# Kernel tuning notes

Hardware: AMD Instinct MI355X
Metric: run time of the kernel (lower is better)

The kernel has to match this reference:

```python
import jax, jax.numpy as jnp
import numpy as np

N = 1048576   # total nodes
B = 32768     # number of graphs
F = 128       # input_dim
STEPS = 6


def setup_inputs() -> dict:
    key = jax.random.key(0)
    k0, k1, k2, k3, k4 = jax.random.split(key, 5)
    s = 1.0 / np.sqrt(F)  # torch LSTM init scale
    x = jax.random.normal(k0, (N, F), dtype=jnp.float32)
    # equal-sized, sorted graph assignment so every graph is non-empty
    batch = (jnp.arange(N, dtype=jnp.int64) * B) // N
    W_ih = jax.random.uniform(k1, (4 * F, 2 * F), jnp.float32, -s, s)
    W_hh = jax.random.uniform(k2, (4 * F, F), jnp.float32, -s, s)
    b_ih = jax.random.uniform(k3, (4 * F,), jnp.float32, -s, s)
    b_hh = jax.random.uniform(k4, (4 * F,), jnp.float32, -s, s)
    return {"x": x, "batch": batch, "W_ih": W_ih, "W_hh": W_hh,
            "b_ih": b_ih, "b_hh": b_hh}


def _lstm_cell(x_in, h, c, W_ih, W_hh, b_ih, b_hh):
    # torch gate order: i, f, g, o
    gates = x_in @ W_ih.T + h @ W_hh.T + b_ih + b_hh  # [B, 4F]
    i, f, g, o = jnp.split(gates, 4, axis=-1)
    c_new = jax.nn.sigmoid(f) * c + jax.nn.sigmoid(i) * jnp.tanh(g)
    h_new = jax.nn.sigmoid(o) * jnp.tanh(c_new)
    return h_new, c_new


def reference(x, batch, W_ih, W_hh, b_ih, b_hh):
    # Vectorized set2set: each graph's batch-1 LSTM is independent, so we run
    # all B graphs' LSTMs as one batched cell, and do the softmax-attention
    # readout with segment ops over the ragged node sets.
    h = jnp.zeros((B, F), x.dtype)
    c = jnp.zeros((B, F), x.dtype)
    q_star = jnp.zeros((B, 2 * F), x.dtype)
    batch = batch.astype(jnp.int32)
    for _ in range(STEPS):
        q, c = _lstm_cell(q_star, h, c, W_ih, W_hh, b_ih, b_hh)  # [B, F]
        h = q
        e = jnp.sum(x * q[batch], axis=-1)  # [N] attention logits
        # per-graph stable softmax
        emax = jax.ops.segment_max(e, batch, num_segments=B)
        ee = jnp.exp(e - emax[batch])
        denom = jax.ops.segment_sum(ee, batch, num_segments=B)
        a = ee / denom[batch]  # [N]
        r = jax.ops.segment_sum(a[:, None] * x, batch, num_segments=B)  # [B, F]
        q_star = jnp.concatenate([q, r], axis=-1)  # [B, 2F]
    return q_star
```

## Files before the change

kernel.cpp:

```cpp
#include <hip/hip_runtime.h>
#include <hip/hip_bf16.h>
#include <hip/hip_fp16.h>
#include <cstdint>


#define NSTEPS   6
#define NSEG     32768
#define NCHUNK   32768
#define MAXC     8
#define XSH      136
#define MTHREADS 1024
#define MGRID    256
#define ESHIFT   20.0f

typedef _Float16 half2_t __attribute__((ext_vector_type(2)));

__device__ __forceinline__ float sigmoidf_(float v) {
    return 1.0f / (1.0f + __expf(-v));
}

__device__ __forceinline__ float fdot2_(unsigned int w, unsigned int q, float acc) {
    return __builtin_amdgcn_fdot2(__builtin_bit_cast(half2_t, w),
                                  __builtin_bit_cast(half2_t, q), acc, false);
}

__device__ __forceinline__ void lgkm_barrier() {
    asm volatile("s_waitcnt lgkmcnt(0)" ::: "memory");
    __builtin_amdgcn_s_barrier();
    asm volatile("" ::: "memory");
}

__global__ void pack_weights_kernel(const float* __restrict__ Wih,
                                    const float* __restrict__ Whh,
                                    const float* __restrict__ bih,
                                    const float* __restrict__ bhh,
                                    float* __restrict__ wtp,
                                    float* __restrict__ b4) {
    const int k = blockIdx.x;
    const int f = threadIdx.x;
    float w[4];
    #pragma unroll
    for (int j = 0; j < 4; ++j) {
        const int row = j * 128 + f;
        float v = Wih[row * 256 + k];
        if (k < 128) v += Whh[row * 128 + k];
        w[j] = v;
    }
    float4 wv; wv.x = w[0]; wv.y = w[1]; wv.z = w[2]; wv.w = w[3];
    reinterpret_cast<float4*>(wtp)[k * 128 + f] = wv;
    if (k == 0) {
        float4 bv;
        bv.x = bih[0 * 128 + f] + bhh[0 * 128 + f];
        bv.y = bih[1 * 128 + f] + bhh[1 * 128 + f];
        bv.z = bih[2 * 128 + f] + bhh[2 * 128 + f];
        bv.w = bih[3 * 128 + f] + bhh[3 * 128 + f];
        reinterpret_cast<float4*>(b4)[f] = bv;
    }
}

__global__ void pack_f16_kernel(const float* __restrict__ wtp,
                                uint4* __restrict__ wph) {
    const int p = blockIdx.x;
    const int f = threadIdx.x;
    const float4 w0 = reinterpret_cast<const float4*>(wtp)[(2 * p) * 128 + f];
    const float4 w1 = reinterpret_cast<const float4*>(wtp)[(2 * p + 1) * 128 + f];
    __half2 h[4];
    h[0] = __floats2half2_rn(w0.x, w1.x);
    h[1] = __floats2half2_rn(w0.y, w1.y);
    h[2] = __floats2half2_rn(w0.z, w1.z);
    h[3] = __floats2half2_rn(w0.w, w1.w);
    wph[p * 128 + f] = *reinterpret_cast<uint4*>(h);
}

__global__ void zero_kernel(int* __restrict__ p, int n) {
    for (int i = blockIdx.x * blockDim.x + threadIdx.x; i < n;
         i += gridDim.x * blockDim.x) p[i] = 0;
}

__global__ void seg_count_kernel(const int* __restrict__ batch,
                                 int* __restrict__ counts) {
    const int c = blockIdx.x * blockDim.x + threadIdx.x;
    if (c < NCHUNK) {
        const int v = batch[c * 32];
        if (v >= 0 && v < NSEG)
            atomicAdd(&counts[v], 1);
    }
}

__global__ __launch_bounds__(1024)
void scan_kernel(const int* __restrict__ counts,
                 int* __restrict__ offs, int* __restrict__ cursor,
                 int* __restrict__ activeList, int* __restrict__ nActive) {
    __shared__ int sc[1024];
    const int t = threadIdx.x;
    const int base = t * 32;
    int local[32];
    int sum = 0;
    #pragma unroll
    for (int j = 0; j < 32; ++j) { local[j] = counts[base + j]; sum += local[j]; }
    sc[t] = sum;
    __syncthreads();
    for (int d = 1; d < 1024; d <<= 1) {
        const int v = (t >= d) ? sc[t - d] : 0;
        __syncthreads();
        sc[t] += v;
        __syncthreads();
    }
    int run = sc[t] - sum;
    for (int j = 0; j < 32; ++j) {
        const int s = base + j;
        offs[s] = run;
        cursor[s] = run;
        if (local[j] > 0) {
            const int idx = atomicAdd(nActive, 1);
            activeList[idx] = s;
        }
        run += local[j];
    }
}

__global__ void fill_kernel(const int* __restrict__ batch,
                            int* __restrict__ cursor,
                            int* __restrict__ chunk_list) {
    const int c = blockIdx.x * blockDim.x + threadIdx.x;
    if (c < NCHUNK) {
        const int v = batch[c * 32];
        if (v >= 0 && v < NSEG) {
            const int pos = atomicAdd(&cursor[v], 1);
            chunk_list[pos] = c;
        }
    }
}

__global__ __launch_bounds__(128)
void empty_traj_kernel(const float* __restrict__ wtp,
                       const float* __restrict__ b4,
                       float* __restrict__ qe,
                       float* __restrict__ qe01) {
    __shared__ float q_s[128];
    const int f = threadIdx.x;
    const float4 bb = reinterpret_cast<const float4*>(b4)[f];
    q_s[f] = 0.0f;
    float c = 0.0f;
    __syncthreads();
    for (int step = 0; step < NSTEPS; ++step) {
        float a0 = 0.f, a1 = 0.f, a2 = 0.f, a3 = 0.f;
        for (int k = 0; k < 128; ++k) {
            const float4 w = reinterpret_cast<const float4*>(wtp)[k * 128 + f];
            const float qv = q_s[k];
            a0 = fmaf(w.x, qv, a0); a1 = fmaf(w.y, qv, a1);
            a2 = fmaf(w.z, qv, a2); a3 = fmaf(w.w, qv, a3);
        }
        __syncthreads();
        c = sigmoidf_(a1 + bb.y) * c + sigmoidf_(a0 + bb.x) * tanhf(a2 + bb.z);
        const float qv = sigmoidf_(a3 + bb.w) * tanhf(c);
        q_s[f] = qv;
        if (step == 0) { qe01[f] = qv; qe01[128 + f] = c; }
        __syncthreads();
    }
    qe[f] = q_s[f];
}

__global__ void bcast_empty_kernel(const int* __restrict__ counts,
                                   const float* __restrict__ qe,
                                   float* __restrict__ out) {
    const int lane = threadIdx.x & 63;
    const int wave0 = (blockIdx.x * blockDim.x + threadIdx.x) >> 6;
    const int nwave = (gridDim.x * blockDim.x) >> 6;
    float4 v = make_float4(0.f, 0.f, 0.f, 0.f);
    if (lane < 32) v = reinterpret_cast<const float4*>(qe)[lane];
    for (int s = wave0; s < NSEG; s += nwave) {
        if (counts[s] != 0) continue;
        reinterpret_cast<float4*>(out)[(size_t)s * 64 + lane] = v;
    }
}

__global__ __launch_bounds__(MTHREADS)
void main_seg_kernel(const float* __restrict__ x,
                     const uint4* __restrict__ wph,
                     const float* __restrict__ b4,
                     const float* __restrict__ qe01,
                     const int* __restrict__ counts,
                     const int* __restrict__ offs,
                     const int* __restrict__ chunk_list,
                     const int* __restrict__ activeList,
                     const int* __restrict__ nActive,
                     float* __restrict__ out) {
    __shared__ __align__(16) __half x_h[2][256][XSH];
    __shared__ __align__(16) __half q_h[2][2][256];
    __shared__ __align__(16) float  e_s[2][256];
    __shared__ __align__(16) float  rpart_s[2][8][128];
    __shared__ float dsum_s[16];
    __shared__ int   clist_s[2][MAXC];
    __shared__ int   cnt_s[2];

    const int t  = threadIdx.x;
    const int ko = t & 7;
    const int f  = t >> 3;
    const float4 bb = reinterpret_cast<const float4*>(b4)[f];
    const float c1v = qe01[128 + f];
    const int nAct  = *nActive;
    const int nPair = (nAct + 1) >> 1;

    uint4 p0, p1, p2, p3;
    {
        int pb = ko * 2;
        asm volatile("" : "+v"(pb));
        p0 = wph[(pb +  0) * 128 + f];
        p1 = wph[(pb +  1) * 128 + f];
        p2 = wph[(pb + 16) * 128 + f];
        p3 = wph[(pb + 17) * 128 + f];
    }

    for (int pp = blockIdx.x; pp < nPair; pp += gridDim.x) {
        if (t < 2) {
            const int idx = 2 * pp + t;
            int cnt = 0;
            if (idx < nAct) {
                const int sseg = activeList[idx];
                cnt = counts[sseg];
                if (cnt > MAXC) cnt = MAXC;
                const int off = offs[sseg];
                for (int j = 0; j < cnt; ++j) clist_s[t][j] = chunk_list[off + j];
                for (int a = 1; a < cnt; ++a) {
                    const int key = clist_s[t][a];
                    int b = a - 1;
                    while (b >= 0 && clist_s[t][b] > key) {
                        clist_s[t][b + 1] = clist_s[t][b]; --b;
                    }
                    clist_s[t][b + 1] = key;
                }
            }
            cnt_s[t] = cnt;
        }
        if (t < 256) q_h[1][t >> 7][t & 127] = __float2half(qe01[t & 127]);
        __syncthreads();
        const int cnt0 = cnt_s[0], cnt1 = cnt_s[1];
        const int nv0 = cnt0 * 32, nv1 = cnt1 * 32;

        #pragma unroll
        for (int sg = 0; sg < 2; ++sg) {
            const int cnt = (sg == 0) ? cnt0 : cnt1;
            for (int p = t; p < cnt * 1024; p += MTHREADS) {
                const int j = p >> 10, g = p & 1023;
                const int row = g >> 5, c4 = g & 31;
                const float4 v = reinterpret_cast<const float4*>(x)
                                    [(size_t)clist_s[sg][j] * 1024 + g];
                __half2* dst =
                    reinterpret_cast<__half2*>(&x_h[sg][j * 32 + row][c4 * 4]);
                dst[0] = __floats2half2_rn(v.x, v.y);
                dst[1] = __floats2half2_rn(v.z, v.w);
            }
            if (cnt < MAXC) {
                const int base = cnt * 32;
                const int nh2 = (256 - base) * (XSH / 2);
                for (int p = t; p < nh2; p += MTHREADS) {
                    const int row = base + p / (XSH / 2);
                    const int cc  = p % (XSH / 2);
                    reinterpret_cast<__half2*>(&x_h[sg][row][0])[cc] =
                        __floats2half2_rn(0.f, 0.f);
                }
            }
        }
        float creg0 = c1v, creg1 = c1v;
        __syncthreads();

        for (int step = 0; step < NSTEPS; ++step) {
            const int cur = step & 1, nxt = cur ^ 1;

            if (step > 0) {
                float a00 = 0.f, a01 = 0.f, a02 = 0.f, a03 = 0.f;
                float a10 = 0.f, a11 = 0.f, a12 = 0.f, a13 = 0.f;
                {
                    const __half* qh0 = &q_h[cur][0][0];
                    const __half* qh1 = &q_h[cur][1][0];
                    int pb = ko * 2;
                    asm volatile("" : "+v"(pb));
                    uint4 c0 = p0, c1 = p1, n0 = p2, n1 = p3;
                    #pragma unroll
                    for (int m = 0; m < 8; ++m) {
                        const uint2 qp0 =
                            *reinterpret_cast<const uint2*>(&qh0[m * 32 + ko * 4]);
                        const uint2 qp1 =
                            *reinterpret_cast<const uint2*>(&qh1[m * 32 + ko * 4]);
                        const uint4 wa = c0, wb = c1;
                        c0 = n0; c1 = n1;
                        if (m < 6) {
                            n0 = wph[(pb + (m + 2) * 16 + 0) * 128 + f];
                            n1 = wph[(pb + (m + 2) * 16 + 1) * 128 + f];
                        }
                        a00 = fdot2_(wa.x, qp0.x, a00); a01 = fdot2_(wa.y, qp0.x, a01);
                        a02 = fdot2_(wa.z, qp0.x, a02); a03 = fdot2_(wa.w, qp0.x, a03);
                        a00 = fdot2_(wb.x, qp0.y, a00); a01 = fdot2_(wb.y, qp0.y, a01);
                        a02 = fdot2_(wb.z, qp0.y, a02); a03 = fdot2_(wb.w, qp0.y, a03);
                        a10 = fdot2_(wa.x, qp1.x, a10); a11 = fdot2_(wa.y, qp1.x, a11);
                        a12 = fdot2_(wa.z, qp1.x, a12); a13 = fdot2_(wa.w, qp1.x, a13);
                        a10 = fdot2_(wb.x, qp1.y, a10); a11 = fdot2_(wb.y, qp1.y, a11);
                        a12 = fdot2_(wb.z, qp1.y, a12); a13 = fdot2_(wb.w, qp1.y, a13);
                    }
                    int pb2 = ko * 2;
                    asm volatile("" : "+v"(pb2));
                    p0 = wph[(pb2 +  0) * 128 + f];
                    p1 = wph[(pb2 +  1) * 128 + f];
                    p2 = wph[(pb2 + 16) * 128 + f];
                    p3 = wph[(pb2 + 17) * 128 + f];
                }
                a00 += __shfl_xor(a00,1); a00 += __shfl_xor(a00,2); a00 += __shfl_xor(a00,4);
                a01 += __shfl_xor(a01,1); a01 += __shfl_xor(a01,2); a01 += __shfl_xor(a01,4);
                a02 += __shfl_xor(a02,1); a02 += __shfl_xor(a02,2); a02 += __shfl_xor(a02,4);
                a03 += __shfl_xor(a03,1); a03 += __shfl_xor(a03,2); a03 += __shfl_xor(a03,4);
                a10 += __shfl_xor(a10,1); a10 += __shfl_xor(a10,2); a10 += __shfl_xor(a10,4);
                a11 += __shfl_xor(a11,1); a11 += __shfl_xor(a11,2); a11 += __shfl_xor(a11,4);
                a12 += __shfl_xor(a12,1); a12 += __shfl_xor(a12,2); a12 += __shfl_xor(a12,4);
                a13 += __shfl_xor(a13,1); a13 += __shfl_xor(a13,2); a13 += __shfl_xor(a13,4);
                if (ko == 0) {
                    {
                        const float gi = a00 + bb.x, gf = a01 + bb.y;
                        const float gg = a02 + bb.z, go = a03 + bb.w;
                        creg0 = sigmoidf_(gf) * creg0 + sigmoidf_(gi) * tanhf(gg);
                        q_h[nxt][0][f] = __float2half(sigmoidf_(go) * tanhf(creg0));
                    }
                    {
                        const float gi = a10 + bb.x, gf = a11 + bb.y;
                        const float gg = a12 + bb.z, go = a13 + bb.w;
                        creg1 = sigmoidf_(gf) * creg1 + sigmoidf_(gi) * tanhf(gg);
                        q_h[nxt][1][f] = __float2half(sigmoidf_(go) * tanhf(creg1));
                    }
                }
                lgkm_barrier();
            }

            {
                const int w  = t >> 6;
                const int l  = t & 63;
                const int sg = w >> 3;
                const int nlo = (w & 7) * 32;
                const int nv = (sg == 0) ? nv0 : nv1;
                const int n  = nlo + (l >> 1);
                const int kh = l & 1;
                const uint4* xr =
                    reinterpret_cast<const uint4*>(&x_h[sg][n][kh * 64]);
                const uint4* qr =
                    reinterpret_cast<const uint4*>(&q_h[nxt][sg][kh * 64]);
                float part = 0.f;
                #pragma unroll
                for (int kk = 0; kk < 8; ++kk) {
                    const uint4 xv = xr[kk];
                    const uint4 qv = qr[kk];
                    part = fdot2_(xv.x, qv.x, part);
                    part = fdot2_(xv.y, qv.y, part);
                    part = fdot2_(xv.z, qv.z, part);
                    part = fdot2_(xv.w, qv.w, part);
                }
                part += __shfl_xor(part, 1);
                const float p = (n < nv) ? __expf(part - ESHIFT) : 0.f;
                if (kh == 0) e_s[sg][n] = p;
                float ws = (kh == 0) ? p : 0.f;
                ws += __shfl_xor(ws, 2);  ws += __shfl_xor(ws, 4);
                ws += __shfl_xor(ws, 8);  ws += __shfl_xor(ws, 16);
                ws += __shfl_xor(ws, 32);
                if (l == 0) dsum_s[w] = ws;
                const int g = l >> 4;
                const int i = l & 15;
                float r0=0.f,r1=0.f,r2=0.f,r3=0.f,r4=0.f,r5=0.f,r6=0.f,r7=0.f;
                #pragma unroll
                for (int j = 0; j < 8; ++j) {
                    const int node = nlo + j * 4 + g;
                    const float pj = e_s[sg][node];
                    const uint4 xv =
                        *reinterpret_cast<const uint4*>(&x_h[sg][node][i * 8]);
                    const float2 f0 = __half22float2(__builtin_bit_cast(__half2, xv.x));
                    const float2 f1 = __half22float2(__builtin_bit_cast(__half2, xv.y));
                    const float2 f2 = __half22float2(__builtin_bit_cast(__half2, xv.z));
                    const float2 f3 = __half22float2(__builtin_bit_cast(__half2, xv.w));
                    r0 = fmaf(pj, f0.x, r0); r1 = fmaf(pj, f0.y, r1);
                    r2 = fmaf(pj, f1.x, r2); r3 = fmaf(pj, f1.y, r3);
                    r4 = fmaf(pj, f2.x, r4); r5 = fmaf(pj, f2.y, r5);
                    r6 = fmaf(pj, f3.x, r6); r7 = fmaf(pj, f3.y, r7);
                }
                r0 += __shfl_xor(r0,16); r0 += __shfl_xor(r0,32);
                r1 += __shfl_xor(r1,16); r1 += __shfl_xor(r1,32);
                r2 += __shfl_xor(r2,16); r2 += __shfl_xor(r2,32);
                r3 += __shfl_xor(r3,16); r3 += __shfl_xor(r3,32);
                r4 += __shfl_xor(r4,16); r4 += __shfl_xor(r4,32);
                r5 += __shfl_xor(r5,16); r5 += __shfl_xor(r5,32);
                r6 += __shfl_xor(r6,16); r6 += __shfl_xor(r6,32);
                r7 += __shfl_xor(r7,16); r7 += __shfl_xor(r7,32);
                if (l < 16) {
                    float4 v0; v0.x=r0; v0.y=r1; v0.z=r2; v0.w=r3;
                    float4 v1; v1.x=r4; v1.y=r5; v1.z=r6; v1.w=r7;
                    *reinterpret_cast<float4*>(&rpart_s[sg][w & 7][i * 8])     = v0;
                    *reinterpret_cast<float4*>(&rpart_s[sg][w & 7][i * 8 + 4]) = v1;
                }
            }
            lgkm_barrier();

            if (t < 256) {
                const int sg = t >> 7, fr = t & 127;
                float den = 0.f;
                #pragma unroll
                for (int j = 0; j < 8; ++j) den += dsum_s[sg * 8 + j];
                float rsum = 0.f;
                #pragma unroll
                for (int j = 0; j < 8; ++j) rsum += rpart_s[sg][j][fr];
                q_h[nxt][sg][128 + fr] = __float2half(rsum / den);
            }
            lgkm_barrier();
        }

        if (t < 512) {
            const int sg = t >> 8, i = t & 255;
            const int idx = 2 * pp + sg;
            if (idx < nAct) {
                const int sseg = activeList[idx];
                out[(size_t)sseg * 256 + i] = __half2float(q_h[0][sg][i]);
            }
        }
        __syncthreads();
    }
}

extern "C" void kernel_launch(void* const* d_in, const int* in_sizes, int n_in,
                              void* d_out, int out_size, void* d_ws, size_t ws_size,
                              hipStream_t stream) {
    (void)in_sizes; (void)n_in; (void)out_size; (void)ws_size;
    const float* x    = (const float*)d_in[0];
    const int*   batch = (const int*)d_in[1];
    const float* Wih  = (const float*)d_in[2];
    const float* Whh  = (const float*)d_in[3];
    const float* bih  = (const float*)d_in[4];
    const float* bhh  = (const float*)d_in[5];
    float* out = (float*)d_out;

    float* wtp       = (float*)d_ws;
    float* b4        = wtp + 131072;
    float* qe        = b4 + 512;
    float* qe01      = qe + 128;
    uint4* wph       = (uint4*)(qe01 + 256);
    int*   counts    = (int*)(wph + 128 * 128);
    int*   offs      = counts + NSEG;
    int*   cursor    = offs + NSEG;
    int*   chunk_lst = cursor + NSEG;
    int*   activeLst = chunk_lst + NCHUNK;
    int*   nActive   = activeLst + NSEG;

    pack_weights_kernel<<<256, 128, 0, stream>>>(Wih, Whh, bih, bhh, wtp, b4);
    pack_f16_kernel<<<128, 128, 0, stream>>>(wtp, wph);
    zero_kernel<<<64, 256, 0, stream>>>(counts, NSEG);
    zero_kernel<<<1, 64, 0, stream>>>(nActive, 1);
    seg_count_kernel<<<NCHUNK / 256, 256, 0, stream>>>(batch, counts);
    scan_kernel<<<1, 1024, 0, stream>>>(counts, offs, cursor, activeLst, nActive);
    fill_kernel<<<NCHUNK / 256, 256, 0, stream>>>(batch, cursor, chunk_lst);
    empty_traj_kernel<<<1, 128, 0, stream>>>(wtp, b4, qe, qe01);
    bcast_empty_kernel<<<512, 256, 0, stream>>>(counts, qe, out);
    main_seg_kernel<<<MGRID, MTHREADS, 0, stream>>>(
        x, wph, b4, qe01, counts, offs, chunk_lst, activeLst, nActive, out);
}
```

Measured before the change: 375.4 us.

## Interleave LSTM gate matvec with attention phases and drop readout partial buffer

Restructures the per-step loop so the gate matrix-vector products for the next step are split into four chunks and interleaved with the attention logits, softmax weights and readout phases of the current step. This hides weight-fetch latency behind shared-memory work. The readout is reorganised so each wave owns a 16-column slice across all nodes and reduces fully with shuffles, which removes the rpart_s buffer and its separate reduction phase and barrier. The q_h buffer indexing and output buffer selection change to match the new step ordering. It risks more register pressure and longer shuffle chains.

```diff
diff --git a/kernel.cpp b/kernel.cpp
--- a/kernel.cpp
+++ b/kernel.cpp
@@ -189,7 +189,6 @@
     __shared__ __align__(16) __half x_h[2][256][XSH];
     __shared__ __align__(16) __half q_h[2][2][256];
     __shared__ __align__(16) float  e_s[2][256];
-    __shared__ __align__(16) float  rpart_s[2][8][128];
     __shared__ float dsum_s[16];
     __shared__ int   clist_s[2][MAXC];
     __shared__ int   cnt_s[2];
@@ -201,6 +200,12 @@
     const float c1v = qe01[128 + f];
     const int nAct  = *nActive;
     const int nPair = (nAct + 1) >> 1;
+
+    const int we  = t >> 6, le = t & 63;
+    const int sgE = we >> 3, nE = (we & 7) * 32 + (le >> 1), khE = le & 1;
+    const int sgR = sgE, cbR = (we & 7) * 16;
+    const int irR = le & 1, gR = le >> 1;
+    const int colh = cbR + irR * 8;
 
     uint4 p0, p1, p2, p3;
     {
@@ -233,10 +238,10 @@
             }
             cnt_s[t] = cnt;
         }
-        if (t < 256) q_h[1][t >> 7][t & 127] = __float2half(qe01[t & 127]);
+        if (t < 256) q_h[0][t >> 7][t & 127] = __float2half(qe01[t & 127]);
         __syncthreads();
         const int cnt0 = cnt_s[0], cnt1 = cnt_s[1];
-        const int nv0 = cnt0 * 32, nv1 = cnt1 * 32;
+        const int nvE = ((sgE == 0) ? cnt0 : cnt1) * 32;
 
         #pragma unroll
         for (int sg = 0; sg < 2; ++sg) {
@@ -265,45 +270,186 @@
         float creg0 = c1v, creg1 = c1v;
         __syncthreads();
 
-        for (int step = 0; step < NSTEPS; ++step) {
-            const int cur = step & 1, nxt = cur ^ 1;
-
-            if (step > 0) {
-                float a00 = 0.f, a01 = 0.f, a02 = 0.f, a03 = 0.f;
-                float a10 = 0.f, a11 = 0.f, a12 = 0.f, a13 = 0.f;
+        for (int s = 0; s < NSTEPS; ++s) {
+            const int cur = s & 1, nxt = cur ^ 1;
+            const bool doGate = (s < NSTEPS - 1);
+            float a00 = 0.f, a01 = 0.f, a02 = 0.f, a03 = 0.f;
+            float a10 = 0.f, a11 = 0.f, a12 = 0.f, a13 = 0.f;
+            const __half* qh0 = &q_h[cur][0][0];
+            const __half* qh1 = &q_h[cur][1][0];
+
+            if (doGate) {
+                #pragma unroll
+                for (int m = 0; m < 2; ++m) {
+                    const uint2 qp0 =
+                        *reinterpret_cast<const uint2*>(&qh0[m * 32 + ko * 4]);
+                    const uint2 qp1 =
+                        *reinterpret_cast<const uint2*>(&qh1[m * 32 + ko * 4]);
+                    const uint4 wa = (m == 0) ? p0 : p2;
+                    const uint4 wb = (m == 0) ? p1 : p3;
+                    a00 = fdot2_(wa.x, qp0.x, a00); a01 = fdot2_(wa.y, qp0.x, a01);
+                    a02 = fdot2_(wa.z, qp0.x, a02); a03 = fdot2_(wa.w, qp0.x, a03);
+                    a00 = fdot2_(wb.x, qp0.y, a00); a01 = fdot2_(wb.y, qp0.y, a01);
+                    a02 = fdot2_(wb.z, qp0.y, a02); a03 = fdot2_(wb.w, qp0.y, a03);
+                    a10 = fdot2_(wa.x, qp1.x, a10); a11 = fdot2_(wa.y, qp1.x, a11);
+                    a12 = fdot2_(wa.z, qp1.x, a12); a13 = fdot2_(wa.w, qp1.x, a13);
+                    a10 = fdot2_(wb.x, qp1.y, a10); a11 = fdot2_(wb.y, qp1.y, a11);
+                    a12 = fdot2_(wb.z, qp1.y, a12); a13 = fdot2_(wb.w, qp1.y, a13);
+                }
+                int pb = ko * 2;
+                asm volatile("" : "+v"(pb));
+                p0 = wph[(pb + 2 * 16 + 0) * 128 + f];
+                p1 = wph[(pb + 2 * 16 + 1) * 128 + f];
+                p2 = wph[(pb + 3 * 16 + 0) * 128 + f];
+                p3 = wph[(pb + 3 * 16 + 1) * 128 + f];
+            }
+
+            {
+                const uint4* xr =
+                    reinterpret_cast<const uint4*>(&x_h[sgE][nE][khE * 64]);
+                const uint4* qr =
+                    reinterpret_cast<const uint4*>(&q_h[cur][sgE][khE * 64]);
+                float part = 0.f;
+                #pragma unroll
+                for (int kk = 0; kk < 8; ++kk) {
+                    const uint4 xv = xr[kk];
+                    const uint4 qv = qr[kk];
+                    part = fdot2_(xv.x, qv.x, part);
+                    part = fdot2_(xv.y, qv.y, part);
+                    part = fdot2_(xv.z, qv.z, part);
+                    part = fdot2_(xv.w, qv.w, part);
+                }
+                part += __shfl_xor(part, 1);
+                const float p = (nE < nvE) ? __expf(part - ESHIFT) : 0.f;
+                if (khE == 0) e_s[sgE][nE] = p;
+                float ws = (khE == 0) ? p : 0.f;
+                ws += __shfl_xor(ws, 2);  ws += __shfl_xor(ws, 4);
+                ws += __shfl_xor(ws, 8);  ws += __shfl_xor(ws, 16);
+                ws += __shfl_xor(ws, 32);
+                if (le == 0) dsum_s[we] = ws;
+            }
+
+            if (doGate) {
+                #pragma unroll
+                for (int m = 2; m < 4; ++m) {
+                    const uint2 qp0 =
+                        *reinterpret_cast<const uint2*>(&qh0[m * 32 + ko * 4]);
+                    const uint2 qp1 =
+                        *reinterpret_cast<const uint2*>(&qh1[m * 32 + ko * 4]);
+                    const uint4 wa = (m == 2) ? p0 : p2;
+                    const uint4 wb = (m == 2) ? p1 : p3;
+                    a00 = fdot2_(wa.x, qp0.x, a00); a01 = fdot2_(wa.y, qp0.x, a01);
+                    a02 = fdot2_(wa.z, qp0.x, a02); a03 = fdot2_(wa.w, qp0.x, a03);
+                    a00 = fdot2_(wb.x, qp0.y, a00); a01 = fdot2_(wb.y, qp0.y, a01);
+                    a02 = fdot2_(wb.z, qp0.y, a02); a03 = fdot2_(wb.w, qp0.y, a03);
+                    a10 = fdot2_(wa.x, qp1.x, a10); a11 = fdot2_(wa.y, qp1.x, a11);
+                    a12 = fdot2_(wa.z, qp1.x, a12); a13 = fdot2_(wa.w, qp1.x, a13);
+                    a10 = fdot2_(wb.x, qp1.y, a10); a11 = fdot2_(wb.y, qp1.y, a11);
+                    a12 = fdot2_(wb.z, qp1.y, a12); a13 = fdot2_(wb.w, qp1.y, a13);
+                }
+                int pb = ko * 2;
+                asm volatile("" : "+v"(pb));
+                p0 = wph[(pb + 4 * 16 + 0) * 128 + f];
+                p1 = wph[(pb + 4 * 16 + 1) * 128 + f];
+                p2 = wph[(pb + 5 * 16 + 0) * 128 + f];
+                p3 = wph[(pb + 5 * 16 + 1) * 128 + f];
+            }
+            lgkm_barrier();
+
+            {
+                float r0=0.f,r1=0.f,r2=0.f,r3=0.f,r4=0.f,r5=0.f,r6=0.f,r7=0.f;
+                #pragma unroll
+                for (int j = 0; j < 8; ++j) {
+                    const int node = gR + j * 32;
+                    const float pj = e_s[sgR][node];
+                    const uint4 xv =
+                        *reinterpret_cast<const uint4*>(&x_h[sgR][node][colh]);
+                    const float2 f0 = __half22float2(__builtin_bit_cast(__half2, xv.x));
+                    const float2 f1 = __half22float2(__builtin_bit_cast(__half2, xv.y));
+                    const float2 f2 = __half22float2(__builtin_bit_cast(__half2, xv.z));
+                    const float2 f3 = __half22float2(__builtin_bit_cast(__half2, xv.w));
+                    r0 = fmaf(pj, f0.x, r0); r1 = fmaf(pj, f0.y, r1);
+                    r2 = fmaf(pj, f1.x, r2); r3 = fmaf(pj, f1.y, r3);
+                    r4 = fmaf(pj, f2.x, r4); r5 = fmaf(pj, f2.y, r5);
+                    r6 = fmaf(pj, f3.x, r6); r7 = fmaf(pj, f3.y, r7);
+                }
+                r0 += __shfl_xor(r0,2); r0 += __shfl_xor(r0,4); r0 += __shfl_xor(r0,8); r0 += __shfl_xor(r0,16); r0 += __shfl_xor(r0,32);
+                r1 += __shfl_xor(r1,2); r1 += __shfl_xor(r1,4); r1 += __shfl_xor(r1,8); r1 += __shfl_xor(r1,16); r1 += __shfl_xor(r1,32);
+                r2 += __shfl_xor(r2,2); r2 += __shfl_xor(r2,4); r2 += __shfl_xor(r2,8); r2 += __shfl_xor(r2,16); r2 += __shfl_xor(r2,32);
+                r3 += __shfl_xor(r3,2); r3 += __shfl_xor(r3,4); r3 += __shfl_xor(r3,8); r3 += __shfl_xor(r3,16); r3 += __shfl_xor(r3,32);
+                r4 += __shfl_xor(r4,2); r4 += __shfl_xor(r4,4); r4 += __shfl_xor(r4,8); r4 += __shfl_xor(r4,16); r4 += __shfl_xor(r4,32);
+                r5 += __shfl_xor(r5,2); r5 += __shfl_xor(r5,4); r5 += __shfl_xor(r5,8); r5 += __shfl_xor(r5,16); r5 += __shfl_xor(r5,32);
+                r6 += __shfl_xor(r6,2); r6 += __shfl_xor(r6,4); r6 += __shfl_xor(r6,8); r6 += __shfl_xor(r6,16); r6 += __shfl_xor(r6,32);
+                r7 += __shfl_xor(r7,2); r7 += __shfl_xor(r7,4); r7 += __shfl_xor(r7,8); r7 += __shfl_xor(r7,16); r7 += __shfl_xor(r7,32);
+                if (le < 2) {
+                    float den = 0.f;
+                    #pragma unroll
+                    for (int j = 0; j < 8; ++j) den += dsum_s[sgR * 8 + j];
+                    const float inv = 1.0f / den;
+                    __half2 h0 = __floats2half2_rn(r0 * inv, r1 * inv);
+                    __half2 h1 = __floats2half2_rn(r2 * inv, r3 * inv);
+                    __half2 h2 = __floats2half2_rn(r4 * inv, r5 * inv);
+                    __half2 h3 = __floats2half2_rn(r6 * inv, r7 * inv);
+                    uint4 pk;
+                    pk.x = __builtin_bit_cast(unsigned int, h0);
+                    pk.y = __builtin_bit_cast(unsigned int, h1);
+                    pk.z = __builtin_bit_cast(unsigned int, h2);
+                    pk.w = __builtin_bit_cast(unsigned int, h3);
+                    *reinterpret_cast<uint4*>(&q_h[cur][sgR][128 + colh]) = pk;
+                }
+            }
+            lgkm_barrier();
+
+            if (doGate) {
+                #pragma unroll
+                for (int m = 4; m < 6; ++m) {
+                    const uint2 qp0 =
+                        *reinterpret_cast<const uint2*>(&qh0[m * 32 + ko * 4]);
+                    const uint2 qp1 =
+                        *reinterpret_cast<const uint2*>(&qh1[m * 32 + ko * 4]);
+                    const uint4 wa = (m == 4) ? p0 : p2;
+                    const uint4 wb = (m == 4) ? p1 : p3;
+                    a00 = fdot2_(wa.x, qp0.x, a00); a01 = fdot2_(wa.y, qp0.x, a01);
+                    a02 = fdot2_(wa.z, qp0.x, a02); a03 = fdot2_(wa.w, qp0.x, a03);
+                    a00 = fdot2_(wb.x, qp0.y, a00); a01 = fdot2_(wb.y, qp0.y, a01);
+                    a02 = fdot2_(wb.z, qp0.y, a02); a03 = fdot2_(wb.w, qp0.y, a03);
+                    a10 = fdot2_(wa.x, qp1.x, a10); a11 = fdot2_(wa.y, qp1.x, a11);
+                    a12 = fdot2_(wa.z, qp1.x, a12); a13 = fdot2_(wa.w, qp1.x, a13);
+                    a10 = fdot2_(wb.x, qp1.y, a10); a11 = fdot2_(wb.y, qp1.y, a11);
+                    a12 = fdot2_(wb.z, qp1.y, a12); a13 = fdot2_(wb.w, qp1.y, a13);
+                }
                 {
-                    const __half* qh0 = &q_h[cur][0][0];
-                    const __half* qh1 = &q_h[cur][1][0];
                     int pb = ko * 2;
                     asm volatile("" : "+v"(pb));
-                    uint4 c0 = p0, c1 = p1, n0 = p2, n1 = p3;
-                    #pragma unroll
-                    for (int m = 0; m < 8; ++m) {
-                        const uint2 qp0 =
-                            *reinterpret_cast<const uint2*>(&qh0[m * 32 + ko * 4]);
-                        const uint2 qp1 =
-                            *reinterpret_cast<const uint2*>(&qh1[m * 32 + ko * 4]);
-                        const uint4 wa = c0, wb = c1;
-                        c0 = n0; c1 = n1;
-                        if (m < 6) {
-                            n0 = wph[(pb + (m + 2) * 16 + 0) * 128 + f];
-                            n1 = wph[(pb + (m + 2) * 16 + 1) * 128 + f];
-                        }
-                        a00 = fdot2_(wa.x, qp0.x, a00); a01 = fdot2_(wa.y, qp0.x, a01);
-                        a02 = fdot2_(wa.z, qp0.x, a02); a03 = fdot2_(wa.w, qp0.x, a03);
-                        a00 = fdot2_(wb.x, qp0.y, a00); a01 = fdot2_(wb.y, qp0.y, a01);
-                        a02 = fdot2_(wb.z, qp0.y, a02); a03 = fdot2_(wb.w, qp0.y, a03);
-                        a10 = fdot2_(wa.x, qp1.x, a10); a11 = fdot2_(wa.y, qp1.x, a11);
-                        a12 = fdot2_(wa.z, qp1.x, a12); a13 = fdot2_(wa.w, qp1.x, a13);
-                        a10 = fdot2_(wb.x, qp1.y, a10); a11 = fdot2_(wb.y, qp1.y, a11);
-                        a12 = fdot2_(wb.z, qp1.y, a12); a13 = fdot2_(wb.w, qp1.y, a13);
-                    }
-                    int pb2 = ko * 2;
-                    asm volatile("" : "+v"(pb2));
-                    p0 = wph[(pb2 +  0) * 128 + f];
-                    p1 = wph[(pb2 +  1) * 128 + f];
-                    p2 = wph[(pb2 + 16) * 128 + f];
-                    p3 = wph[(pb2 + 17) * 128 + f];
+                    p0 = wph[(pb + 6 * 16 + 0) * 128 + f];
+                    p1 = wph[(pb + 6 * 16 + 1) * 128 + f];
+                    p2 = wph[(pb + 7 * 16 + 0) * 128 + f];
+                    p3 = wph[(pb + 7 * 16 + 1) * 128 + f];
+                }
+                #pragma unroll
+                for (int m = 6; m < 8; ++m) {
+                    const uint2 qp0 =
+                        *reinterpret_cast<const uint2*>(&qh0[m * 32 + ko * 4]);
+                    const uint2 qp1 =
+                        *reinterpret_cast<const uint2*>(&qh1[m * 32 + ko * 4]);
+                    const uint4 wa = (m == 6) ? p0 : p2;
+                    const uint4 wb = (m == 6) ? p1 : p3;
+                    a00 = fdot2_(wa.x, qp0.x, a00); a01 = fdot2_(wa.y, qp0.x, a01);
+                    a02 = fdot2_(wa.z, qp0.x, a02); a03 = fdot2_(wa.w, qp0.x, a03);
+                    a00 = fdot2_(wb.x, qp0.y, a00); a01 = fdot2_(wb.y, qp0.y, a01);
+                    a02 = fdot2_(wb.z, qp0.y, a02); a03 = fdot2_(wb.w, qp0.y, a03);
+                    a10 = fdot2_(wa.x, qp1.x, a10); a11 = fdot2_(wa.y, qp1.x, a11);
+                    a12 = fdot2_(wa.z, qp1.x, a12); a13 = fdot2_(wa.w, qp1.x, a13);
+                    a10 = fdot2_(wb.x, qp1.y, a10); a11 = fdot2_(wb.y, qp1.y, a11);
+                    a12 = fdot2_(wb.z, qp1.y, a12); a13 = fdot2_(wb.w, qp1.y, a13);
+                }
+                {
+                    int pb = ko * 2;
+                    asm volatile("" : "+v"(pb));
+                    p0 = wph[(pb +  0) * 128 + f];
+                    p1 = wph[(pb +  1) * 128 + f];
+                    p2 = wph[(pb + 16) * 128 + f];
+                    p3 = wph[(pb + 17) * 128 + f];
                 }
                 a00 += __shfl_xor(a00,1); a00 += __shfl_xor(a00,2); a00 += __shfl_xor(a00,4);
                 a01 += __shfl_xor(a01,1); a01 += __shfl_xor(a01,2); a01 += __shfl_xor(a01,4);
@@ -327,83 +473,6 @@
                         q_h[nxt][1][f] = __float2half(sigmoidf_(go) * tanhf(creg1));
                     }
                 }
-                lgkm_barrier();
-            }
-
-            {
-                const int w  = t >> 6;
-                const int l  = t & 63;
-                const int sg = w >> 3;
-                const int nlo = (w & 7) * 32;
-                const int nv = (sg == 0) ? nv0 : nv1;
-                const int n  = nlo + (l >> 1);
-                const int kh = l & 1;
-                const uint4* xr =
-                    reinterpret_cast<const uint4*>(&x_h[sg][n][kh * 64]);
-                const uint4* qr =
-                    reinterpret_cast<const uint4*>(&q_h[nxt][sg][kh * 64]);
-                float part = 0.f;
-                #pragma unroll
-                for (int kk = 0; kk < 8; ++kk) {
-                    const uint4 xv = xr[kk];
-                    const uint4 qv = qr[kk];
-                    part = fdot2_(xv.x, qv.x, part);
-                    part = fdot2_(xv.y, qv.y, part);
-                    part = fdot2_(xv.z, qv.z, part);
-                    part = fdot2_(xv.w, qv.w, part);
-                }
-                part += __shfl_xor(part, 1);
-                const float p = (n < nv) ? __expf(part - ESHIFT) : 0.f;
-                if (kh == 0) e_s[sg][n] = p;
-                float ws = (kh == 0) ? p : 0.f;
-                ws += __shfl_xor(ws, 2);  ws += __shfl_xor(ws, 4);
-                ws += __shfl_xor(ws, 8);  ws += __shfl_xor(ws, 16);
-                ws += __shfl_xor(ws, 32);
-                if (l == 0) dsum_s[w] = ws;
-                const int g = l >> 4;
-                const int i = l & 15;
-                float r0=0.f,r1=0.f,r2=0.f,r3=0.f,r4=0.f,r5=0.f,r6=0.f,r7=0.f;
-                #pragma unroll
-                for (int j = 0; j < 8; ++j) {
-                    const int node = nlo + j * 4 + g;
-                    const float pj = e_s[sg][node];
-                    const uint4 xv =
-                        *reinterpret_cast<const uint4*>(&x_h[sg][node][i * 8]);
-                    const float2 f0 = __half22float2(__builtin_bit_cast(__half2, xv.x));
-                    const float2 f1 = __half22float2(__builtin_bit_cast(__half2, xv.y));
-                    const float2 f2 = __half22float2(__builtin_bit_cast(__half2, xv.z));
-                    const float2 f3 = __half22float2(__builtin_bit_cast(__half2, xv.w));
-                    r0 = fmaf(pj, f0.x, r0); r1 = fmaf(pj, f0.y, r1);
-                    r2 = fmaf(pj, f1.x, r2); r3 = fmaf(pj, f1.y, r3);
-                    r4 = fmaf(pj, f2.x, r4); r5 = fmaf(pj, f2.y, r5);
-                    r6 = fmaf(pj, f3.x, r6); r7 = fmaf(pj, f3.y, r7);
-                }
-                r0 += __shfl_xor(r0,16); r0 += __shfl_xor(r0,32);
-                r1 += __shfl_xor(r1,16); r1 += __shfl_xor(r1,32);
-                r2 += __shfl_xor(r2,16); r2 += __shfl_xor(r2,32);
-                r3 += __shfl_xor(r3,16); r3 += __shfl_xor(r3,32);
-                r4 += __shfl_xor(r4,16); r4 += __shfl_xor(r4,32);
-                r5 += __shfl_xor(r5,16); r5 += __shfl_xor(r5,32);
-                r6 += __shfl_xor(r6,16); r6 += __shfl_xor(r6,32);
-                r7 += __shfl_xor(r7,16); r7 += __shfl_xor(r7,32);
-                if (l < 16) {
-                    float4 v0; v0.x=r0; v0.y=r1; v0.z=r2; v0.w=r3;
-                    float4 v1; v1.x=r4; v1.y=r5; v1.z=r6; v1.w=r7;
-                    *reinterpret_cast<float4*>(&rpart_s[sg][w & 7][i * 8])     = v0;
-                    *reinterpret_cast<float4*>(&rpart_s[sg][w & 7][i * 8 + 4]) = v1;
-                }
-            }
-            lgkm_barrier();
-
-            if (t < 256) {
-                const int sg = t >> 7, fr = t & 127;
-                float den = 0.f;
-                #pragma unroll
-                for (int j = 0; j < 8; ++j) den += dsum_s[sg * 8 + j];
-                float rsum = 0.f;
-                #pragma unroll
-                for (int j = 0; j < 8; ++j) rsum += rpart_s[sg][j][fr];
-                q_h[nxt][sg][128 + fr] = __float2half(rsum / den);
             }
             lgkm_barrier();
         }
@@ -413,7 +482,7 @@
             const int idx = 2 * pp + sg;
             if (idx < nAct) {
                 const int sseg = activeList[idx];
-                out[(size_t)sseg * 256 + i] = __half2float(q_h[0][sg][i]);
+                out[(size_t)sseg * 256 + i] = __half2float(q_h[1][sg][i]);
             }
         }
         __syncthreads();
```

Result: no change. 375.1 us (-0.1%).
